# Kernel tuning notes

Measured on AMD Instinct MI355X. Metric: run time of the kernel, lower is better.

## Reference

```python
import math
import jax, jax.numpy as jnp
import numpy as np

NUM_HEADS = 12
HEAD_DIM = 64
HIDDEN = NUM_HEADS * HEAD_DIM  # 768
SEQ = 4096


def setup_inputs() -> dict:
    key = jax.random.key(0)
    ks = jax.random.split(key, 7)
    s = 0.02  # BERT-style init scale for weights
    return {
        "hidden_states": jax.random.normal(ks[0], (1, SEQ, HIDDEN), jnp.float32),
        "Wq": jax.random.normal(ks[1], (HIDDEN, HIDDEN), jnp.float32) * s,
        "bq": jax.random.normal(ks[2], (HIDDEN,), jnp.float32) * s,
        "Wk": jax.random.normal(ks[3], (HIDDEN, HIDDEN), jnp.float32) * s,
        "bk": jax.random.normal(ks[4], (HIDDEN,), jnp.float32) * s,
        "Wv": jax.random.normal(ks[5], (HIDDEN, HIDDEN), jnp.float32) * s,
        "bv": jax.random.normal(ks[6], (HIDDEN,), jnp.float32) * s,
    }


def _split_heads(z):
    # [S, HIDDEN] -> [H, S, dh]
    S = z.shape[0]
    return jnp.transpose(z.reshape(S, NUM_HEADS, HEAD_DIM), (1, 0, 2))


def reference(hidden_states, Wq, bq, Wk, bk, Wv, bv):
    # batch is squeezed in the original module (kernel is unbatched)
    x = hidden_states[0]  # [S, D]
    q = _split_heads(x @ Wq.T + bq)  # [H, S, dh]
    k = _split_heads(x @ Wk.T + bk)  # [H, S, dh]
    scale = 1.0 / math.sqrt(HEAD_DIM)
    scores = jnp.einsum('hqd,hkd->hqk', q, k) * scale  # [H, S, S]
    probs = jax.nn.softmax(scores, axis=-1)
    # multi_rand_attn_cuda approximates P @ (x @ Wv^T + bv) via CDF-driven
    # Monte-Carlo column sampling of Wv; its expectation is the exact product,
    # which is the correctness baseline computed here.
    v = _split_heads(x @ Wv.T + bv)  # [H, S, dh]
    ctx = jnp.einsum('hqk,hkd->hqd', probs, v)  # [H, S, dh]
    ctx = jnp.transpose(ctx, (1, 0, 2)).reshape(x.shape[0], HIDDEN)
    return ctx[None]  # [1, S, D]
```

## Files before the change

### kernel.cpp

```cpp
#include <hip/hip_runtime.h>
#include <stdint.h>


typedef float    f32x4 __attribute__((ext_vector_type(4)));
typedef _Float16 h16x8 __attribute__((ext_vector_type(8)));
typedef _Float16 h16x4 __attribute__((ext_vector_type(4)));
typedef _Float16 h16x2 __attribute__((ext_vector_type(2)));
typedef __fp16   fp16x2 __attribute__((ext_vector_type(2)));
typedef unsigned short u16;

#define MFMA32(A, B, C) __builtin_amdgcn_mfma_f32_16x16x32_f16((A), (B), (C), 0, 0, 0)
#define MFMA16(A, B, C) __builtin_amdgcn_mfma_f32_16x16x16f16((A), (B), (C), 0, 0, 0)
#define ZERO4 ((f32x4){0.f, 0.f, 0.f, 0.f})

#define SEQ 4096
#define HID 768
#define NH  12
#define DH  64

#define CEXP 0.18033688011112042f

__device__ __forceinline__ u16 f2h(float f) {
  union { _Float16 h; u16 u; } v;
  v.h = (_Float16)f;
  return v.u;
}
__device__ __forceinline__ float h2f(u16 u) {
  union { u16 u; _Float16 h; } v;
  v.u = u;
  return (float)v.h;
}

__device__ __forceinline__ void gload_lds16(const void* g, void* l) {
  __builtin_amdgcn_global_load_lds(
      (__attribute__((address_space(1))) void*)(g),
      (__attribute__((address_space(3))) void*)(l),
      16, 0, 0);
}

__global__ __launch_bounds__(256) void cast_all_k(
    const float* __restrict__ x,  const float* __restrict__ wq,
    const float* __restrict__ wk, const float* __restrict__ wv,
    u16* __restrict__ xh,  u16* __restrict__ wqh,
    u16* __restrict__ wkh, u16* __restrict__ wvh)
{
  int i = blockIdx.x * 256 + threadIdx.x;
  const int NX4 = (SEQ * HID) / 4;
  const int NW4 = (HID * HID) / 4;
  const float4* src; ushort4* dst; int idx;
  if (i < NX4) {
    src = (const float4*)x; dst = (ushort4*)xh; idx = i;
  } else {
    int j = i - NX4;
    int w = j / NW4;
    idx = j - w * NW4;
    src = (const float4*)(w == 0 ? wq : (w == 1 ? wk : wv));
    dst = (ushort4*)(w == 0 ? wqh : (w == 1 ? wkh : wvh));
  }
  float4 v = src[idx];
  ushort4 o;
  o.x = f2h(v.x); o.y = f2h(v.y); o.z = f2h(v.z); o.w = f2h(v.w);
  dst[idx] = o;
}

__global__ __launch_bounds__(256, 3) void qkv_gemm_k(
    const u16* __restrict__ xh,
    const u16* __restrict__ wqh, const u16* __restrict__ wkh, const u16* __restrict__ wvh,
    const float* __restrict__ bq, const float* __restrict__ bk, const float* __restrict__ bv,
    u16* __restrict__ Qh, u16* __restrict__ Kh, u16* __restrict__ Vt)
{
  __shared__ u16 As[128 * 32];
  __shared__ u16 Bs[128 * 32];

  const int t = threadIdx.x;
  const int wave = t >> 6, lane = t & 63;
  const int m = lane & 15, quad = lane >> 4;
  const int z  = blockIdx.z;
  const int n0 = blockIdx.x * 128;
  const int m0 = blockIdx.y * 128;

  const u16*   W    = (z == 0) ? wqh : (z == 1) ? wkh : wvh;
  const float* bias = (z == 0) ? bq  : (z == 1) ? bk  : bv;

  const int wm = (wave >> 1) * 64;
  const int wn = (wave & 1) * 64;

  f32x4 acc[4][4];
#pragma unroll
  for (int i = 0; i < 4; i++)
#pragma unroll
    for (int j = 0; j < 4; j++) acc[i][j] = ZERO4;

  const int srow = t >> 2;
  const int sch  = t & 3;
  const u16* gA = xh + (m0 + srow) * HID + sch * 8;
  const u16* gB = W  + (n0 + srow) * HID + sch * 8;
  u16* lA = As + wave * 512;
  u16* lB = Bs + wave * 512;

  for (int k0 = 0; k0 < HID; k0 += 32) {
    __syncthreads();
#pragma unroll
    for (int c = 0; c < 2; c++) {
      gload_lds16(gA + c * 64 * HID + k0, lA + c * 2048);
      gload_lds16(gB + c * 64 * HID + k0, lB + c * 2048);
    }
    __syncthreads();

    h16x8 af[4], bf[4];
#pragma unroll
    for (int i = 0; i < 4; i++)
      af[i] = *(const h16x8*)(As + (wm + i * 16 + m) * 32 + quad * 8);
#pragma unroll
    for (int j = 0; j < 4; j++)
      bf[j] = *(const h16x8*)(Bs + (wn + j * 16 + m) * 32 + quad * 8);
#pragma unroll
    for (int i = 0; i < 4; i++)
#pragma unroll
      for (int j = 0; j < 4; j++)
        acc[i][j] = MFMA32(af[i], bf[j], acc[i][j]);
  }

  if (z < 2) {
    u16* outp = (z == 0) ? Qh : Kh;
    const float sc = (z == 0) ? CEXP : 1.0f;
#pragma unroll
    for (int i = 0; i < 4; i++) {
      int row = m0 + wm + i * 16 + quad * 4;
#pragma unroll
      for (int j = 0; j < 4; j++) {
        int col = n0 + wn + j * 16 + m;
        float bb = bias[col];
#pragma unroll
        for (int r = 0; r < 4; r++)
          outp[(row + r) * HID + col] = f2h((acc[i][j][r] + bb) * sc);
      }
    }
  } else {
#pragma unroll
    for (int i = 0; i < 4; i++) {
      int row = m0 + wm + i * 16 + quad * 4;
#pragma unroll
      for (int j = 0; j < 4; j++) {
        int col = n0 + wn + j * 16 + m;
        float bb = bias[col];
        ushort4 o;
        o.x = f2h(acc[i][j][0] + bb);
        o.y = f2h(acc[i][j][1] + bb);
        o.z = f2h(acc[i][j][2] + bb);
        o.w = f2h(acc[i][j][3] + bb);
        int vrow = row ^ ((col & 8) ? 4 : 0);
        *(ushort4*)(Vt + col * SEQ + vrow) = o;
      }
    }
  }
}

__global__ __launch_bounds__(256, 3) void attn_k(
    const u16* __restrict__ Qh, const u16* __restrict__ Kh, const u16* __restrict__ Vt,
    float* __restrict__ out0, u16* __restrict__ Op1, float* __restrict__ Lp)
{
  __shared__ u16 Ks[128 * 64];
  __shared__ u16 Vs[64 * 128];

  const int t = threadIdx.x;
  const int wave = t >> 6, lane = t & 63;
  const int m = lane & 15, quad = lane >> 4;
  const int h  = blockIdx.y;
  const int q0 = blockIdx.x * 128;
  const int sp = blockIdx.z;
  const int kvbase = sp * 2048;

  h16x8 qf[2][2];
#pragma unroll
  for (int qn = 0; qn < 2; qn++)
#pragma unroll
    for (int ks = 0; ks < 2; ks++)
      qf[qn][ks] = *(const h16x8*)(Qh + (q0 + wave * 32 + qn * 16 + m) * HID
                                   + h * DH + ks * 32 + quad * 8);

  f32x4 O[2][4];
#pragma unroll
  for (int qn = 0; qn < 2; qn++)
#pragma unroll
    for (int jd = 0; jd < 4; jd++) O[qn][jd] = ZERO4;
  float lsum[2] = {0.f, 0.f};

  const int krow_b = wave * 8 + (lane >> 3);
  const int kcl    = lane & 7;
  const int vrow_b = wave * 4 + (lane >> 4);
  const int vcl    = lane & 15;
  const int vsub   = ((quad & 1) ^ ((m >> 3) & 1)) * 4;

  for (int it = 0; it < 16; ++it) {
    const int kv0 = kvbase + it * 128;
    __syncthreads();
#pragma unroll
    for (int c = 0; c < 4; c++) {
      int row = c * 32 + krow_b;
      int cg  = kcl ^ (row & 7);
      gload_lds16(Kh + (kv0 + row) * HID + h * DH + cg * 8,
                  Ks + c * 2048 + wave * 512);
      int d  = c * 16 + vrow_b;
      int vg = vcl ^ (d & 15);
      gload_lds16(Vt + (h * DH + d) * SEQ + kv0 + vg * 8,
                  Vs + c * 2048 + wave * 512);
    }
    __syncthreads();

#pragma unroll
    for (int j = 0; j < 8; ++j) {
      const int krow = j * 16 + m;
      h16x8 kb0 = *(const h16x8*)(Ks + krow * 64 + ((quad    ) ^ (m & 7)) * 8);
      h16x8 kb1 = *(const h16x8*)(Ks + krow * 64 + ((4 + quad) ^ (m & 7)) * 8);

      f32x4 S[2];
#pragma unroll
      for (int qn = 0; qn < 2; qn++) {
        S[qn] = MFMA32(kb0, qf[qn][0], ZERO4);
        S[qn] = MFMA32(kb1, qf[qn][1], S[qn]);
      }

      h16x4 vb[4];
#pragma unroll
      for (int jd = 0; jd < 4; jd++) {
        int d = jd * 16 + m;
        vb[jd] = *(const h16x4*)(Vs + d * 128
                                 + (((j * 2 + (quad >> 1)) ^ m) * 8) + vsub);
      }

#pragma unroll
      for (int qn = 0; qn < 2; qn++) {
        float e0 = __builtin_amdgcn_exp2f(S[qn][0]);
        float e1 = __builtin_amdgcn_exp2f(S[qn][1]);
        float e2 = __builtin_amdgcn_exp2f(S[qn][2]);
        float e3 = __builtin_amdgcn_exp2f(S[qn][3]);
        lsum[qn] += (e0 + e1) + (e2 + e3);
        fp16x2 p01 = __builtin_amdgcn_cvt_pkrtz(e0, e1);
        fp16x2 p23 = __builtin_amdgcn_cvt_pkrtz(e2, e3);
        h16x2 q01 = __builtin_bit_cast(h16x2, p01);
        h16x2 q23 = __builtin_bit_cast(h16x2, p23);
        h16x4 pa  = __builtin_shufflevector(q01, q23, 0, 1, 2, 3);
#pragma unroll
        for (int jd = 0; jd < 4; jd++)
          O[qn][jd] = MFMA16(pa, vb[jd], O[qn][jd]);
      }
    }
  }

#pragma unroll
  for (int qn = 0; qn < 2; qn++) {
    float v = lsum[qn];
    v += __shfl_xor(v, 16, 64);
    v += __shfl_xor(v, 32, 64);
    if (quad == 0)
      Lp[sp * NH * SEQ + h * SEQ + q0 + wave * 32 + qn * 16 + m] = v;
#pragma unroll
    for (int jd = 0; jd < 4; jd++) {
      int col = h * DH + jd * 16 + m;
#pragma unroll
      for (int r = 0; r < 4; r++) {
        int row = q0 + wave * 32 + qn * 16 + quad * 4 + r;
        if (sp == 0) out0[row * HID + col] = O[qn][jd][r];
        else         Op1[row * HID + col] = f2h(O[qn][jd][r]);
      }
    }
  }
}

__global__ __launch_bounds__(256) void reduce_k(
    float* __restrict__ out, const u16* __restrict__ Op1,
    const float* __restrict__ Lp)
{
  int i = blockIdx.x * 256 + threadIdx.x;
  int s  = i / 192;
  int c4 = i - s * 192;
  int h  = c4 >> 4;
  float L = Lp[h * SEQ + s] + Lp[NH * SEQ + h * SEQ + s];
  float inv = __builtin_amdgcn_rcpf(L);
  float4 a = ((const float4*)out)[i];
  ushort4 b = ((const ushort4*)Op1)[i];
  float4 r;
  r.x = (a.x + h2f(b.x)) * inv;
  r.y = (a.y + h2f(b.y)) * inv;
  r.z = (a.z + h2f(b.z)) * inv;
  r.w = (a.w + h2f(b.w)) * inv;
  ((float4*)out)[i] = r;
}

extern "C" void kernel_launch(void* const* d_in, const int* in_sizes, int n_in,
                              void* d_out, int out_size, void* d_ws, size_t ws_size,
                              hipStream_t stream) {
  const float* x  = (const float*)d_in[0];
  const float* Wq = (const float*)d_in[1];
  const float* bq = (const float*)d_in[2];
  const float* Wk = (const float*)d_in[3];
  const float* bk = (const float*)d_in[4];
  const float* Wv = (const float*)d_in[5];
  const float* bv = (const float*)d_in[6];
  float* out = (float*)d_out;

  char* ws = (char*)d_ws;
  u16* Qh  = (u16*)(ws);
  u16* Kh  = (u16*)(ws + 6291456);
  u16* Vt  = (u16*)(ws + 12582912);
  u16* xh  = (u16*)(ws + 18874368);
  u16* wqh = (u16*)(ws + 25165824);
  u16* wkh = (u16*)(ws + 26345472);
  u16* wvh = (u16*)(ws + 27525120);
  u16*   Op1 = (u16*)(ws + 18874368);
  float* Lp  = (float*)(ws + 25165824);

  cast_all_k<<<4800, 256, 0, stream>>>(x, Wq, Wk, Wv, xh, wqh, wkh, wvh);
  qkv_gemm_k<<<dim3(6, 32, 3), 256, 0, stream>>>(xh, wqh, wkh, wvh,
                                                 bq, bk, bv, Qh, Kh, Vt);
  attn_k<<<dim3(32, NH, 2), 256, 0, stream>>>(Qh, Kh, Vt, out, Op1, Lp);
  reduce_k<<<3072, 256, 0, stream>>>(out, Op1, Lp);
}
```

Before: 177.0 us.

## Use 16x16x32 MFMA for PV and deepen QKV GEMM K-tile with swizzle

The attention PV product now processes two 16-key score tiles at once, packing eight probabilities per lane so it can use the 16x16x32 f16 MFMA instead of 16x16x16. The V-transpose layout written by the QKV GEMM is permuted to match the new 8-element V fragment reads. The QKV GEMM also moves from a 32-wide to a 64-wide K tile with an XOR-swizzled LDS layout, halving loop iterations and barriers. The aim is fewer, denser MFMA instructions and less sync overhead, at the cost of more registers and LDS per block.

```diff
diff --git a/kernel.cpp b/kernel.cpp
--- a/kernel.cpp
+++ b/kernel.cpp
@@ -10,7 +10,6 @@
 typedef unsigned short u16;
 
 #define MFMA32(A, B, C) __builtin_amdgcn_mfma_f32_16x16x32_f16((A), (B), (C), 0, 0, 0)
-#define MFMA16(A, B, C) __builtin_amdgcn_mfma_f32_16x16x16f16((A), (B), (C), 0, 0, 0)
 #define ZERO4 ((f32x4){0.f, 0.f, 0.f, 0.f})
 
 #define SEQ 4096
@@ -69,8 +68,8 @@
     const float* __restrict__ bq, const float* __restrict__ bk, const float* __restrict__ bv,
     u16* __restrict__ Qh, u16* __restrict__ Kh, u16* __restrict__ Vt)
 {
-  __shared__ u16 As[128 * 32];
-  __shared__ u16 Bs[128 * 32];
+  __shared__ u16 As[128 * 64];
+  __shared__ u16 Bs[128 * 64];
 
   const int t = threadIdx.x;
   const int wave = t >> 6, lane = t & 63;
@@ -91,34 +90,39 @@
 #pragma unroll
     for (int j = 0; j < 4; j++) acc[i][j] = ZERO4;
 
-  const int srow = t >> 2;
-  const int sch  = t & 3;
-  const u16* gA = xh + (m0 + srow) * HID + sch * 8;
-  const u16* gB = W  + (n0 + srow) * HID + sch * 8;
+  const int srow = wave * 8 + (lane >> 3);
+  const int scg  = (lane & 7) ^ (srow & 7);
+  const u16* gA = xh + (m0 + srow) * HID + scg * 8;
+  const u16* gB = W  + (n0 + srow) * HID + scg * 8;
   u16* lA = As + wave * 512;
   u16* lB = Bs + wave * 512;
 
-  for (int k0 = 0; k0 < HID; k0 += 32) {
+  for (int k0 = 0; k0 < HID; k0 += 64) {
     __syncthreads();
 #pragma unroll
-    for (int c = 0; c < 2; c++) {
-      gload_lds16(gA + c * 64 * HID + k0, lA + c * 2048);
-      gload_lds16(gB + c * 64 * HID + k0, lB + c * 2048);
+    for (int c = 0; c < 4; c++) {
+      gload_lds16(gA + c * 32 * HID + k0, lA + c * 2048);
+      gload_lds16(gB + c * 32 * HID + k0, lB + c * 2048);
     }
     __syncthreads();
 
-    h16x8 af[4], bf[4];
-#pragma unroll
-    for (int i = 0; i < 4; i++)
-      af[i] = *(const h16x8*)(As + (wm + i * 16 + m) * 32 + quad * 8);
-#pragma unroll
-    for (int j = 0; j < 4; j++)
-      bf[j] = *(const h16x8*)(Bs + (wn + j * 16 + m) * 32 + quad * 8);
-#pragma unroll
-    for (int i = 0; i < 4; i++)
+#pragma unroll
+    for (int s = 0; s < 2; s++) {
+      h16x8 af[4], bf[4];
+#pragma unroll
+      for (int i = 0; i < 4; i++)
+        af[i] = *(const h16x8*)(As + (wm + i * 16 + m) * 64
+                                + ((s * 4 + quad) ^ (m & 7)) * 8);
 #pragma unroll
       for (int j = 0; j < 4; j++)
-        acc[i][j] = MFMA32(af[i], bf[j], acc[i][j]);
+        bf[j] = *(const h16x8*)(Bs + (wn + j * 16 + m) * 64
+                                + ((s * 4 + quad) ^ (m & 7)) * 8);
+#pragma unroll
+      for (int i = 0; i < 4; i++)
+#pragma unroll
+        for (int j = 0; j < 4; j++)
+          acc[i][j] = MFMA32(af[i], bf[j], acc[i][j]);
+    }
   }
 
   if (z < 2) {
@@ -140,6 +144,7 @@
 #pragma unroll
     for (int i = 0; i < 4; i++) {
       int row = m0 + wm + i * 16 + quad * 4;
+      int vpos = (row & ~31) + ((row >> 2) & 3) * 8 + ((row >> 4) & 1) * 4;
 #pragma unroll
       for (int j = 0; j < 4; j++) {
         int col = n0 + wn + j * 16 + m;
@@ -149,8 +154,7 @@
         o.y = f2h(acc[i][j][1] + bb);
         o.z = f2h(acc[i][j][2] + bb);
         o.w = f2h(acc[i][j][3] + bb);
-        int vrow = row ^ ((col & 8) ? 4 : 0);
-        *(ushort4*)(Vt + col * SEQ + vrow) = o;
+        *(ushort4*)(Vt + col * SEQ + vpos) = o;
       }
     }
   }
@@ -190,7 +194,6 @@
   const int kcl    = lane & 7;
   const int vrow_b = wave * 4 + (lane >> 4);
   const int vcl    = lane & 15;
-  const int vsub   = ((quad & 1) ^ ((m >> 3) & 1)) * 4;
 
   for (int it = 0; it < 16; ++it) {
     const int kv0 = kvbase + it * 128;
@@ -209,41 +212,53 @@
     __syncthreads();
 
 #pragma unroll
-    for (int j = 0; j < 8; ++j) {
-      const int krow = j * 16 + m;
-      h16x8 kb0 = *(const h16x8*)(Ks + krow * 64 + ((quad    ) ^ (m & 7)) * 8);
-      h16x8 kb1 = *(const h16x8*)(Ks + krow * 64 + ((4 + quad) ^ (m & 7)) * 8);
-
-      f32x4 S[2];
-#pragma unroll
-      for (int qn = 0; qn < 2; qn++) {
-        S[qn] = MFMA32(kb0, qf[qn][0], ZERO4);
-        S[qn] = MFMA32(kb1, qf[qn][1], S[qn]);
-      }
-
-      h16x4 vb[4];
+    for (int p = 0; p < 4; ++p) {
+      const int krow0 = (2 * p) * 16 + m;
+      const int krow1 = krow0 + 16;
+      h16x8 kb00 = *(const h16x8*)(Ks + krow0 * 64 + ((    quad) ^ (m & 7)) * 8);
+      h16x8 kb01 = *(const h16x8*)(Ks + krow0 * 64 + ((4 + quad) ^ (m & 7)) * 8);
+      h16x8 kb10 = *(const h16x8*)(Ks + krow1 * 64 + ((    quad) ^ (m & 7)) * 8);
+      h16x8 kb11 = *(const h16x8*)(Ks + krow1 * 64 + ((4 + quad) ^ (m & 7)) * 8);
+
+      h16x8 vb[4];
 #pragma unroll
       for (int jd = 0; jd < 4; jd++) {
         int d = jd * 16 + m;
-        vb[jd] = *(const h16x4*)(Vs + d * 128
-                                 + (((j * 2 + (quad >> 1)) ^ m) * 8) + vsub);
+        vb[jd] = *(const h16x8*)(Vs + d * 128 + (((p * 4 + quad) ^ m) * 8));
       }
 
 #pragma unroll
       for (int qn = 0; qn < 2; qn++) {
-        float e0 = __builtin_amdgcn_exp2f(S[qn][0]);
-        float e1 = __builtin_amdgcn_exp2f(S[qn][1]);
-        float e2 = __builtin_amdgcn_exp2f(S[qn][2]);
-        float e3 = __builtin_amdgcn_exp2f(S[qn][3]);
-        lsum[qn] += (e0 + e1) + (e2 + e3);
+        f32x4 S0 = MFMA32(kb00, qf[qn][0], ZERO4);
+        S0       = MFMA32(kb01, qf[qn][1], S0);
+        f32x4 S1 = MFMA32(kb10, qf[qn][0], ZERO4);
+        S1       = MFMA32(kb11, qf[qn][1], S1);
+
+        float e0 = __builtin_amdgcn_exp2f(S0[0]);
+        float e1 = __builtin_amdgcn_exp2f(S0[1]);
+        float e2 = __builtin_amdgcn_exp2f(S0[2]);
+        float e3 = __builtin_amdgcn_exp2f(S0[3]);
+        float e4 = __builtin_amdgcn_exp2f(S1[0]);
+        float e5 = __builtin_amdgcn_exp2f(S1[1]);
+        float e6 = __builtin_amdgcn_exp2f(S1[2]);
+        float e7 = __builtin_amdgcn_exp2f(S1[3]);
+        lsum[qn] += ((e0 + e1) + (e2 + e3)) + ((e4 + e5) + (e6 + e7));
+
         fp16x2 p01 = __builtin_amdgcn_cvt_pkrtz(e0, e1);
         fp16x2 p23 = __builtin_amdgcn_cvt_pkrtz(e2, e3);
+        fp16x2 p45 = __builtin_amdgcn_cvt_pkrtz(e4, e5);
+        fp16x2 p67 = __builtin_amdgcn_cvt_pkrtz(e6, e7);
         h16x2 q01 = __builtin_bit_cast(h16x2, p01);
         h16x2 q23 = __builtin_bit_cast(h16x2, p23);
-        h16x4 pa  = __builtin_shufflevector(q01, q23, 0, 1, 2, 3);
+        h16x2 q45 = __builtin_bit_cast(h16x2, p45);
+        h16x2 q67 = __builtin_bit_cast(h16x2, p67);
+        h16x4 pl = __builtin_shufflevector(q01, q23, 0, 1, 2, 3);
+        h16x4 ph = __builtin_shufflevector(q45, q67, 0, 1, 2, 3);
+        h16x8 pa = __builtin_shufflevector(pl, ph, 0, 1, 2, 3, 4, 5, 6, 7);
+
 #pragma unroll
         for (int jd = 0; jd < 4; jd++)
-          O[qn][jd] = MFMA16(pa, vb[jd], O[qn][jd]);
+          O[qn][jd] = MFMA32(pa, vb[jd], O[qn][jd]);
       }
     }
   }
```

New measurement: 165.5 us. 1.07x faster.
